# Performance work log

Hardware: AMD Instinct MI355X
Metric: run time of the kernel (lower is better)

## Reference

```python
import jax, jax.numpy as jnp
import numpy as np

B, L, DM, H, DH = 2, 2048, 1024, 4, 128
TOT = H * DH  # 512


def _dwconv(x, w, b, L):
    # x: (B,L,C), w: (C,1,4) depthwise, padding=3 then causal trim to L (matches Conv1d(padding=3)[...,:L])
    y = jax.lax.conv_general_dilated(x.transpose(0, 2, 1), w, (1,), [(3, 3)],
                                     dimension_numbers=('NCH', 'OIH', 'NCH'),
                                     feature_group_count=w.shape[0])
    y = y[..., :L] + b[None, :, None]
    return y.transpose(0, 2, 1)


def _l2norm(x):
    return x / jnp.maximum(jnp.linalg.norm(x, axis=-1, keepdims=True), 1e-12)


def setup_inputs() -> dict:
    key = jax.random.key(0)
    ks = jax.random.split(key, 16)
    s = 0.02
    return {
        'x': jax.random.normal(ks[0], (B, L, DM), jnp.float32),
        'state': jnp.zeros((B, H, DH, DH), jnp.float32),
        'Wq': jax.random.normal(ks[1], (TOT, DM), jnp.float32) * s,
        'Wk': jax.random.normal(ks[2], (TOT, DM), jnp.float32) * s,
        'Wv': jax.random.normal(ks[3], (2 * TOT, DM), jnp.float32) * s,
        'Wa': jax.random.normal(ks[4], (H, DM), jnp.float32) * s,
        'Wb': jax.random.normal(ks[5], (H, DM), jnp.float32) * s,
        'Wg': jax.random.normal(ks[6], (TOT, DM), jnp.float32) * s,
        'Wo': jax.random.normal(ks[7], (DM, TOT), jnp.float32) * s,
        'qcw': jax.random.normal(ks[8], (TOT, 1, 4), jnp.float32) * 0.1,
        'qcb': jnp.zeros((TOT,), jnp.float32),
        'kcw': jax.random.normal(ks[9], (TOT, 1, 4), jnp.float32) * 0.1,
        'kcb': jnp.zeros((TOT,), jnp.float32),
        'vcw': jax.random.normal(ks[10], (2 * TOT, 1, 4), jnp.float32) * 0.1,
        'vcb': jnp.zeros((2 * TOT,), jnp.float32),
        'ln_w': jnp.ones((TOT,), jnp.float32),
        'ln_b': jnp.zeros((TOT,), jnp.float32),
    }


def reference(x, state, Wq, Wk, Wv, Wa, Wb, Wg, Wo, qcw, qcb, kcw, kcb, vcw, vcb, ln_w, ln_b):
    Bn, Ln, _ = x.shape
    q = _dwconv(x @ Wq.T, qcw, qcb, Ln)
    k = _dwconv(x @ Wk.T, kcw, kcb, Ln)
    v = _dwconv(x @ Wv.T, vcw, vcb, Ln)
    # silu then L2-normalize over the FULL total_dim (before head split), as in the source
    q = _l2norm(jax.nn.silu(q))
    k = _l2norm(jax.nn.silu(k))
    v = jax.nn.silu(v)
    alpha = jax.nn.sigmoid(x @ Wa.T)  # (B,L,H)
    beta = jax.nn.sigmoid(x @ Wb.T)   # (B,L,H)
    q = q.reshape(Bn, Ln, H, DH)
    k = k.reshape(Bn, Ln, H, DH)
    v_main, v_gate = jnp.split(v, 2, axis=-1)
    v_main = v_main.reshape(Bn, Ln, H, DH)
    v_gate = v_gate.reshape(Bn, Ln, H, DH)

    def step(S, inp):
        q_t, k_t, v_t, a_t, b_t = inp  # (B,H,D),(B,H,D),(B,H,D),(B,H),(B,H)
        a = a_t[..., None, None]
        b = b_t[..., None, None]
        Sk = jnp.einsum('bhij,bhj->bhi', S, k_t)  # S @ k
        # S @ (alpha*(I - beta k k^T)) + beta v k^T, via rank-1 update
        S = a * (S - b * (Sk[..., :, None] * k_t[..., None, :])) \
            + b * (v_t[..., :, None] * k_t[..., None, :])
        o = jnp.einsum('bhij,bhj->bhi', S, q_t)
        return S, o

    xs = (q.transpose(1, 0, 2, 3), k.transpose(1, 0, 2, 3), v_main.transpose(1, 0, 2, 3),
          alpha.transpose(1, 0, 2), beta.transpose(1, 0, 2))
    final_state, outs = jax.lax.scan(step, state, xs)
    out = outs.transpose(1, 0, 2, 3)  # (B,L,H,D)

    out = (out * v_gate).reshape(Bn, Ln, TOT)
    out = out * jax.nn.silu(x @ Wg.T)
    mu = out.mean(-1, keepdims=True)
    var = jnp.mean((out - mu) ** 2, axis=-1, keepdims=True)
    out = (out - mu) * jax.lax.rsqrt(var + 1e-5) * ln_w + ln_b
    out = out @ Wo.T
    return out, final_state
```

## Files before the change

### kernel.cpp

```cpp
#include <hip/hip_runtime.h>
#include <hip/hip_bf16.h>

#define BQ    2
#define LQ    2048
#define DMQ   1024
#define HQ    4
#define DHQ   128
#define TOTQ  512
#define BLQ   4096
#define NPROJ 2688
#define KPROJ 1024
#define CT    64
#define NCH   32

typedef short bf16x8 __attribute__((ext_vector_type(8)));
typedef short s16x4  __attribute__((ext_vector_type(4)));
typedef float f32x4  __attribute__((ext_vector_type(4)));

#define MFMA16(a, b, c) __builtin_amdgcn_mfma_f32_16x16x32_bf16(a, b, c, 0, 0, 0)

__device__ __forceinline__ float siluf(float x) { return x / (1.f + __expf(-x)); }
__device__ __forceinline__ float sigf(float x)  { return 1.f / (1.f + __expf(-x)); }
__device__ __forceinline__ short bf16s(float x) {
  return __builtin_bit_cast(short, __float2bfloat16(x));
}
__device__ __forceinline__ float bfu2f(unsigned short u) {
  return __bfloat162float(__builtin_bit_cast(__hip_bfloat16, u));
}
__device__ __forceinline__ bf16x8 pack8(f32x4 a, f32x4 b) {
  bf16x8 r;
  r[0] = bf16s(a.x); r[1] = bf16s(a.y); r[2] = bf16s(a.z); r[3] = bf16s(a.w);
  r[4] = bf16s(b.x); r[5] = bf16s(b.y); r[6] = bf16s(b.z); r[7] = bf16s(b.w);
  return r;
}

__device__ __forceinline__ void gload_lds16(const void* g, void* l) {
  __builtin_amdgcn_global_load_lds(
      (__attribute__((address_space(1))) void*)(unsigned long long)g,
      (__attribute__((address_space(3))) void*)(unsigned int)(unsigned long long)l,
      16, 0, 0);
}

__global__ __launch_bounds__(256)
void cast_all_kernel(const float* __restrict__ x, const float* __restrict__ Wo,
                     const float* __restrict__ Wq, const float* __restrict__ Wk,
                     const float* __restrict__ Wv, const float* __restrict__ Wg,
                     const float* __restrict__ Wa, const float* __restrict__ Wb,
                     __hip_bfloat16* __restrict__ XB, __hip_bfloat16* __restrict__ WOB,
                     __hip_bfloat16* __restrict__ Wcat)
{
  const int bid = blockIdx.x;
  const int tid = threadIdx.x;
  if (bid < 4096) {
    const int i = bid * 256 + tid;
    float4 v = ((const float4*)x)[i];
    __hip_bfloat16 o[4] = { __float2bfloat16(v.x), __float2bfloat16(v.y),
                            __float2bfloat16(v.z), __float2bfloat16(v.w) };
    *(ushort4*)((unsigned short*)XB + (size_t)i * 4) = *(ushort4*)o;
  } else if (bid < 4608) {
    const int i = (bid - 4096) * 256 + tid;
    float4 v = ((const float4*)Wo)[i];
    __hip_bfloat16 o[4] = { __float2bfloat16(v.x), __float2bfloat16(v.y),
                            __float2bfloat16(v.z), __float2bfloat16(v.w) };
    *(ushort4*)((unsigned short*)WOB + (size_t)i * 4) = *(ushort4*)o;
  } else {
    const int i4 = (bid - 4608) * 256 + tid;
    const int row = i4 >> 8;
    const int col = (i4 & 255) * 4;
    const int idx = row * 1024 + col;
    float4 v;
    if      (row < 512)  v = *(const float4*)(Wq + idx);
    else if (row < 1024) v = *(const float4*)(Wk + idx - 512 * 1024);
    else if (row < 2048) v = *(const float4*)(Wv + idx - 1024 * 1024);
    else if (row < 2560) v = *(const float4*)(Wg + idx - 2048 * 1024);
    else if (row < 2564) v = *(const float4*)(Wa + (row - 2560) * 1024 + col);
    else if (row < 2568) v = *(const float4*)(Wb + (row - 2564) * 1024 + col);
    else                 v = make_float4(0.f, 0.f, 0.f, 0.f);
    __hip_bfloat16 o[4] = { __float2bfloat16(v.x), __float2bfloat16(v.y),
                            __float2bfloat16(v.z), __float2bfloat16(v.w) };
    *(ushort4*)((unsigned short*)Wcat + idx) = *(ushort4*)o;
  }
}

template <typename TOUT>
__global__ __launch_bounds__(256)
void gemm_bt_kernel(const __hip_bfloat16* __restrict__ A,
                    const __hip_bfloat16* __restrict__ Bw,
                    TOUT* __restrict__ C, int M, int N, int K,
                    float* __restrict__ aux, int auxc0)
{
  __shared__ __hip_bfloat16 As[2 * 128 * 32];
  __shared__ __hip_bfloat16 Bs[2 * 128 * 32];
  const int tid  = threadIdx.x;
  const int lane = tid & 63;
  const int w    = tid >> 6;
  const int wm   = w >> 1, wn = w & 1;
  const int tm   = blockIdx.x, tn = blockIdx.y;
  const int lr   = lane & 15, lk = lane >> 4;

  f32x4 acc[4][4] = {};

  const int e0   = tid * 8;
  const int srow = e0 >> 5;
  const int scol = e0 & 31;
  const __hip_bfloat16* Ap = A  + (size_t)(tm * 128 + srow) * K + scol;
  const __hip_bfloat16* Bp = Bw + (size_t)(tn * 128 + srow) * K + scol;
  char* AsB  = (char*)As;
  char* BsB  = (char*)Bs;
  const size_t half = (size_t)64 * K;
  const int nk = K >> 5;

  {
    char* AsD = AsB + w * 1024;
    char* BsD = BsB + w * 1024;
    gload_lds16(Ap,        AsD);
    gload_lds16(Ap + half, AsD + 4096);
    gload_lds16(Bp,        BsD);
    gload_lds16(Bp + half, BsD + 4096);
  }
  __syncthreads();

  for (int it = 0; it < nk; ++it) {
    const int sel = it & 1;
    if (it + 1 < nk) {
      const int kk = (it + 1) * 32;
      char* AsD = AsB + ((sel ^ 1) * 8192) + w * 1024;
      char* BsD = BsB + ((sel ^ 1) * 8192) + w * 1024;
      gload_lds16(Ap + kk,        AsD);
      gload_lds16(Ap + half + kk, AsD + 4096);
      gload_lds16(Bp + kk,        BsD);
      gload_lds16(Bp + half + kk, BsD + 4096);
    }
    const char* AsR = AsB + sel * 8192;
    const char* BsR = BsB + sel * 8192;
    bf16x8 af[4], bfv[4];
#pragma unroll
    for (int m = 0; m < 4; ++m)
      af[m]  = *(const bf16x8*)(AsR + ((wm * 64 + m * 16 + lr) * 32 + lk * 8) * 2);
#pragma unroll
    for (int n = 0; n < 4; ++n)
      bfv[n] = *(const bf16x8*)(BsR + ((wn * 64 + n * 16 + lr) * 32 + lk * 8) * 2);
#pragma unroll
    for (int m = 0; m < 4; ++m)
#pragma unroll
      for (int n = 0; n < 4; ++n)
        acc[m][n] = MFMA16(af[m], bfv[n], acc[m][n]);
    __syncthreads();
  }

  const int crow0 = tm * 128 + wm * 64 + (lane >> 4) * 4;
  const int ccol0 = tn * 128 + wn * 64 + lr;
#pragma unroll
  for (int m = 0; m < 4; ++m)
#pragma unroll
    for (int n = 0; n < 4; ++n) {
      const int cc = ccol0 + n * 16;
#pragma unroll
      for (int j = 0; j < 4; ++j) {
        const float v = acc[m][n][j];
        const size_t row = (size_t)(crow0 + m * 16 + j);
        if constexpr (sizeof(TOUT) == 2)
          ((unsigned short*)C)[row * N + cc] = (unsigned short)bf16s(v);
        else
          C[row * N + cc] = v;
        if (aux && cc >= auxc0 && cc < auxc0 + 8)
          aux[row * 8 + (cc - auxc0)] = v;
      }
    }
}

__global__ __launch_bounds__(256)
void conv_act_kernel(const __hip_bfloat16* __restrict__ C, const float* __restrict__ abf,
                     const float* __restrict__ qcw, const float* __restrict__ qcb,
                     const float* __restrict__ kcw, const float* __restrict__ kcb,
                     const float* __restrict__ vcw, const float* __restrict__ vcb,
                     __hip_bfloat16* __restrict__ qh, __hip_bfloat16* __restrict__ kh,
                     __hip_bfloat16* __restrict__ vm, __hip_bfloat16* __restrict__ vg,
                     float* __restrict__ al, float* __restrict__ be)
{
  const int blk = blockIdx.x;
  const int bl0 = blk * 8;
  const int t0  = bl0 & (LQ - 1);
  const int tid = threadIdx.x;
  const unsigned short* Cu = (const unsigned short*)C;
  __shared__ float red[4][16];

  float2 qv[8], kv[8];
  float sq[8], sk[8];
#pragma unroll
  for (int t = 0; t < 8; ++t) { sq[t] = 0.f; sk[t] = 0.f; }

  {
    const int c0 = tid * 2;
    const float4 wqA = *(const float4*)(qcw + 4 * c0);
    const float4 wqB = *(const float4*)(qcw + 4 * c0 + 4);
    const float4 wkA = *(const float4*)(kcw + 4 * c0);
    const float4 wkB = *(const float4*)(kcw + 4 * c0 + 4);
    const float2 bq = *(const float2*)(qcb + c0);
    const float2 bk = *(const float2*)(kcb + c0);
    float2 wrq[11], wrk[11];
#pragma unroll
    for (int r = 0; r < 11; ++r) {
      const int tt = t0 - 3 + r;
      if (tt >= 0) {
        const unsigned short* Cr = Cu + (size_t)(bl0 - 3 + r) * NPROJ;
        const ushort2 aq = *(const ushort2*)(Cr + c0);
        const ushort2 ak = *(const ushort2*)(Cr + 512 + c0);
        wrq[r] = make_float2(bfu2f(aq.x), bfu2f(aq.y));
        wrk[r] = make_float2(bfu2f(ak.x), bfu2f(ak.y));
      } else {
        wrq[r] = make_float2(0.f, 0.f);
        wrk[r] = make_float2(0.f, 0.f);
      }
    }
#pragma unroll
    for (int t = 0; t < 8; ++t) {
      float aq0 = bq.x, aq1 = bq.y, ak0 = bk.x, ak1 = bk.y;
#pragma unroll
      for (int j = 0; j < 4; ++j) {
        aq0 = fmaf(((const float*)&wqA)[j], wrq[t + j].x, aq0);
        aq1 = fmaf(((const float*)&wqB)[j], wrq[t + j].y, aq1);
        ak0 = fmaf(((const float*)&wkA)[j], wrk[t + j].x, ak0);
        ak1 = fmaf(((const float*)&wkB)[j], wrk[t + j].y, ak1);
      }
      const float q0 = siluf(aq0), q1 = siluf(aq1);
      const float k0 = siluf(ak0), k1 = siluf(ak1);
      qv[t] = make_float2(q0, q1);
      kv[t] = make_float2(k0, k1);
      sq[t] = fmaf(q1, q1, fmaf(q0, q0, sq[t]));
      sk[t] = fmaf(k1, k1, fmaf(k0, k0, sk[t]));
    }
  }
#pragma unroll
  for (int m = 1; m < 64; m <<= 1) {
#pragma unroll
    for (int t = 0; t < 8; ++t) {
      sq[t] += __shfl_xor(sq[t], m);
      sk[t] += __shfl_xor(sk[t], m);
    }
  }
  {
    const int w = tid >> 6, lane = tid & 63;
    if (lane == 0) {
#pragma unroll
      for (int t = 0; t < 8; ++t) { red[w][t] = sq[t]; red[w][8 + t] = sk[t]; }
    }
  }
  __syncthreads();
  float rnq[8], rnk[8];
#pragma unroll
  for (int t = 0; t < 8; ++t) {
    const float SQ = red[0][t] + red[1][t] + red[2][t] + red[3][t];
    const float SK = red[0][8 + t] + red[1][8 + t] + red[2][8 + t] + red[3][8 + t];
    rnq[t] = 1.f / fmaxf(sqrtf(SQ), 1e-12f);
    rnk[t] = 1.f / fmaxf(sqrtf(SK), 1e-12f);
  }
  {
    const int c0 = tid * 2;
#pragma unroll
    for (int t = 0; t < 8; ++t) {
      ushort2 oq, ok;
      oq.x = (unsigned short)bf16s(qv[t].x * rnq[t]);
      oq.y = (unsigned short)bf16s(qv[t].y * rnq[t]);
      ok.x = (unsigned short)bf16s(kv[t].x * rnk[t]);
      ok.y = (unsigned short)bf16s(kv[t].y * rnk[t]);
      *(ushort2*)((unsigned short*)qh + (size_t)(bl0 + t) * 512 + c0) = oq;
      *(ushort2*)((unsigned short*)kh + (size_t)(bl0 + t) * 512 + c0) = ok;
    }
  }
  {
    const int cv = tid * 4;
    const float4 wv0 = *(const float4*)(vcw + 4 * cv);
    const float4 wv1 = *(const float4*)(vcw + 4 * cv + 4);
    const float4 wv2 = *(const float4*)(vcw + 4 * cv + 8);
    const float4 wv3 = *(const float4*)(vcw + 4 * cv + 12);
    const float4 bv4 = *(const float4*)(vcb + cv);
    float4 wr[11];
#pragma unroll
    for (int r = 0; r < 11; ++r) {
      const int tt = t0 - 3 + r;
      if (tt >= 0) {
        const ushort4 u = *(const ushort4*)(Cu + (size_t)(bl0 - 3 + r) * NPROJ + 1024 + cv);
        wr[r] = make_float4(bfu2f(u.x), bfu2f(u.y), bfu2f(u.z), bfu2f(u.w));
      } else {
        wr[r] = make_float4(0.f, 0.f, 0.f, 0.f);
      }
    }
#pragma unroll
    for (int t = 0; t < 8; ++t) {
      float a0 = bv4.x, a1 = bv4.y, a2 = bv4.z, a3 = bv4.w;
#pragma unroll
      for (int j = 0; j < 4; ++j) {
        a0 = fmaf(((const float*)&wv0)[j], ((const float*)&wr[t + j])[0], a0);
        a1 = fmaf(((const float*)&wv1)[j], ((const float*)&wr[t + j])[1], a1);
        a2 = fmaf(((const float*)&wv2)[j], ((const float*)&wr[t + j])[2], a2);
        a3 = fmaf(((const float*)&wv3)[j], ((const float*)&wr[t + j])[3], a3);
      }
      ushort4 o;
      o.x = (unsigned short)bf16s(siluf(a0));
      o.y = (unsigned short)bf16s(siluf(a1));
      o.z = (unsigned short)bf16s(siluf(a2));
      o.w = (unsigned short)bf16s(siluf(a3));
      if (cv < 512) *(ushort4*)((unsigned short*)vm + (size_t)(bl0 + t) * 512 + cv)         = o;
      else          *(ushort4*)((unsigned short*)vg + (size_t)(bl0 + t) * 512 + (cv - 512)) = o;
    }
  }
  if (tid < 64) {
    const int t = tid >> 3;
    const int k = tid & 7;
    const float v = abf[(size_t)(bl0 + t) * 8 + k];
    if (k < 4) al[(size_t)(bl0 + t) * 4 + k]       = sigf(v);
    else       be[(size_t)(bl0 + t) * 4 + (k - 4)] = sigf(v);
  }
}

__global__ __launch_bounds__(512)
void scan_phaseA_kernel(const __hip_bfloat16* __restrict__ qh, const __hip_bfloat16* __restrict__ kh,
                        const __hip_bfloat16* __restrict__ vm, const float* __restrict__ al,
                        const float* __restrict__ be,
                        short* __restrict__ WTB, short* __restrict__ ZB,
                        short* __restrict__ PHB, float* __restrict__ GV,
                        short* __restrict__ TRB, float* __restrict__ BF)
{
  __shared__ char sm[136192];
  float* Xl = (float*)(sm);
  __hip_bfloat16* KBl = (__hip_bfloat16*)(sm);
  __hip_bfloat16* QBl = (__hip_bfloat16*)(sm + 17408);
  float* Ll  = (float*)(sm + 65536);
  float* dv  = (float*)(sm + 82944);
  float* bv  = (float*)(sm + 83200);
  float* gbv = (float*)(sm + 83456);
  float* fvs = (float*)(sm + 83712);
  short* KTl  = (short*)(sm + 83968);
  short* WTFl = (short*)(sm + 101376);
  short* ZFl  = (short*)(sm + 118784);

  const int cb = blockIdx.x;
  const int bh = cb & 7, c = cb >> 3;
  const int b = bh >> 2, h = bh & 3;
  const int tid = threadIdx.x;
  const int lane = tid & 63;
  const int w = tid >> 6;
  const int lr = lane & 15, lk = lane >> 4;
  const size_t rowbase = (size_t)(b * LQ + c * CT) * 512 + h * 128;

#pragma unroll
  for (int rep = 0; rep < 2; ++rep) {
    const int fid = tid + rep * 512;
    const int r = fid >> 4;
    const int cg = (fid & 15) * 8;
    *(bf16x8*)(KBl + r * 136 + cg) = *(const bf16x8*)(kh + rowbase + (size_t)r * 512 + cg);
    *(bf16x8*)(QBl + r * 136 + cg) = *(const bf16x8*)(qh + rowbase + (size_t)r * 512 + cg);
  }
  if (w == 0) {
    float la = __logf(al[(size_t)(b * LQ + c * CT + lane) * 4 + h]);
    const float bb = be[(size_t)(b * LQ + c * CT + lane) * 4 + h];
#pragma unroll
    for (int off = 1; off < 64; off <<= 1) {
      const float tv = __shfl_up(la, off, 64);
      if (lane >= off) la += tv;
    }
    dv[lane] = la; bv[lane] = bb; gbv[lane] = bb * __expf(la);
    const float d63 = __shfl(la, 63, 64);
    fvs[lane] = __expf(d63 - la);
    GV[cb * 64 + lane] = __expf(la);
  }
  __syncthreads();

  {
    const int tb = (w & 3) * 16;
    const int sh = (w >> 2) * 2;
    f32x4 aG[2] = {}, aP[2] = {};
#pragma unroll
    for (int ks = 0; ks < 4; ++ks) {
      bf16x8 bk[2];
#pragma unroll
      for (int nt = 0; nt < 2; ++nt)
        bk[nt] = *(const bf16x8*)(KBl + ((sh + nt) * 16 + lr) * 136 + ks * 32 + lk * 8);
      const bf16x8 ak = *(const bf16x8*)(KBl + (tb + lr) * 136 + ks * 32 + lk * 8);
      const bf16x8 aq = *(const bf16x8*)(QBl + (tb + lr) * 136 + ks * 32 + lk * 8);
#pragma unroll
      for (int nt = 0; nt < 2; ++nt) {
        aG[nt] = MFMA16(ak, bk[nt], aG[nt]);
        aP[nt] = MFMA16(aq, bk[nt], aP[nt]);
      }
    }
#pragma unroll
    for (int nt = 0; nt < 2; ++nt)
#pragma unroll
      for (int jj = 0; jj < 4; ++jj) {
        const int t = tb + lk * 4 + jj;
        const int s = (sh + nt) * 16 + lr;
        const float eg = __expf(dv[t] - dv[s]);
        Ll[t * 68 + s] = (t > s) ? bv[t] * eg * aG[nt][jj] : 0.f;
        PHB[(size_t)cb * 4096 + t * 64 + s] = (s <= t) ? bf16s(eg * aP[nt][jj]) : (short)0;
      }
  }
  if (tid < 128) {
    const short* Kbs = (const short*)KBl;
#pragma unroll
    for (int s4 = 0; s4 < 16; ++s4) {
      s16x4 pk;
#pragma unroll
      for (int e = 0; e < 4; ++e)
        pk[e] = Kbs[(s4 * 4 + e) * 136 + tid];
      *(s16x4*)(KTl + tid * 68 + s4 * 4) = pk;
    }
  }
  __syncthreads();

  const int j = tid & 255;
  const int half = tid >> 8;
  const int i0 = half * 8;
  const __hip_bfloat16* src = (j < 128) ? kh : vm;
  const __hip_bfloat16* xp = src + rowbase + (j & 127);
  float* XlC = Xl + j;
  short* dstN = (j < 128) ? (WTB + (size_t)cb * 8192 + j)
                          : (ZB  + (size_t)cb * 8192 + (j - 128));
  short* dstT = (j < 128) ? (WTFl + j * 68)
                          : (ZFl  + (j - 128) * 68);

  for (int r = 0; r < 4; ++r) {
    float u[8];
#pragma unroll
    for (int i = 0; i < 8; ++i) {
      const int t = r * 16 + i0 + i;
      u[i] = __bfloat162float(xp[(size_t)t * 512]) * ((j < 128) ? gbv[t] : bv[t]);
    }
    for (int sc = 0; sc < r; ++sc) {
      float xs[16];
#pragma unroll
      for (int k = 0; k < 16; ++k) xs[k] = XlC[(sc * 16 + k) * 256];
#pragma unroll
      for (int i = 0; i < 8; ++i) {
        const float* lrow = Ll + (r * 16 + i0 + i) * 68 + sc * 16;
        const f32x4 l0 = *(const f32x4*)(lrow);
        const f32x4 l1 = *(const f32x4*)(lrow + 4);
        const f32x4 l2 = *(const f32x4*)(lrow + 8);
        const f32x4 l3 = *(const f32x4*)(lrow + 12);
        f32x4 acc = {};
        acc.x = fmaf(l0.x, xs[0],  acc.x); acc.y = fmaf(l0.y, xs[1],  acc.y);
        acc.z = fmaf(l0.z, xs[2],  acc.z); acc.w = fmaf(l0.w, xs[3],  acc.w);
        acc.x = fmaf(l1.x, xs[4],  acc.x); acc.y = fmaf(l1.y, xs[5],  acc.y);
        acc.z = fmaf(l1.z, xs[6],  acc.z); acc.w = fmaf(l1.w, xs[7],  acc.w);
        acc.x = fmaf(l2.x, xs[8],  acc.x); acc.y = fmaf(l2.y, xs[9],  acc.y);
        acc.z = fmaf(l2.z, xs[10], acc.z); acc.w = fmaf(l2.w, xs[11], acc.w);
        acc.x = fmaf(l3.x, xs[12], acc.x); acc.y = fmaf(l3.y, xs[13], acc.y);
        acc.z = fmaf(l3.z, xs[14], acc.z); acc.w = fmaf(l3.w, xs[15], acc.w);
        u[i] -= (acc.x + acc.y) + (acc.z + acc.w);
      }
    }
    if (half == 0) {
#pragma unroll
      for (int i = 1; i < 8; ++i) {
        const float* lrow = Ll + (r * 16 + i) * 68 + r * 16;
        f32x4 acc = {};
#pragma unroll
        for (int k4 = 0; k4 < 2; ++k4) {
          if (k4 * 4 < i) {
            const f32x4 lv = *(const f32x4*)(lrow + k4 * 4);
            acc.x = fmaf(lv.x, u[k4 * 4 + 0], acc.x);
            acc.y = fmaf(lv.y, u[k4 * 4 + 1], acc.y);
            acc.z = fmaf(lv.z, u[k4 * 4 + 2], acc.z);
            acc.w = fmaf(lv.w, u[k4 * 4 + 3], acc.w);
          }
        }
        u[i] -= (acc.x + acc.y) + (acc.z + acc.w);
      }
#pragma unroll
      for (int i = 0; i < 8; ++i) XlC[(r * 16 + i) * 256] = u[i];
#pragma unroll
      for (int i = 0; i < 8; ++i) dstN[(r * 16 + i) * 128] = bf16s(u[i]);
#pragma unroll
      for (int s4 = 0; s4 < 2; ++s4) {
        s16x4 p;
#pragma unroll
        for (int e = 0; e < 4; ++e)
          p[e] = bf16s(fvs[r * 16 + s4 * 4 + e] * u[s4 * 4 + e]);
        *(s16x4*)(dstT + r * 16 + s4 * 4) = p;
      }
    }
    __syncthreads();
    if (half == 1) {
      float xa[8];
#pragma unroll
      for (int k = 0; k < 8; ++k) xa[k] = XlC[(r * 16 + k) * 256];
#pragma unroll
      for (int i = 0; i < 8; ++i) {
        const float* lrow = Ll + (r * 16 + 8 + i) * 68 + r * 16;
        const f32x4 l0 = *(const f32x4*)(lrow);
        const f32x4 l1 = *(const f32x4*)(lrow + 4);
        f32x4 acc = {};
        acc.x = fmaf(l0.x, xa[0], acc.x); acc.y = fmaf(l0.y, xa[1], acc.y);
        acc.z = fmaf(l0.z, xa[2], acc.z); acc.w = fmaf(l0.w, xa[3], acc.w);
        acc.x = fmaf(l1.x, xa[4], acc.x); acc.y = fmaf(l1.y, xa[5], acc.y);
        acc.z = fmaf(l1.z, xa[6], acc.z); acc.w = fmaf(l1.w, xa[7], acc.w);
        u[i] -= (acc.x + acc.y) + (acc.z + acc.w);
      }
#pragma unroll
      for (int i = 1; i < 8; ++i) {
        const float* lrow = Ll + (r * 16 + 8 + i) * 68 + r * 16 + 8;
        f32x4 acc = {};
#pragma unroll
        for (int k4 = 0; k4 < 2; ++k4) {
          if (k4 * 4 < i) {
            const f32x4 lv = *(const f32x4*)(lrow + k4 * 4);
            acc.x = fmaf(lv.x, u[k4 * 4 + 0], acc.x);
            acc.y = fmaf(lv.y, u[k4 * 4 + 1], acc.y);
            acc.z = fmaf(lv.z, u[k4 * 4 + 2], acc.z);
            acc.w = fmaf(lv.w, u[k4 * 4 + 3], acc.w);
          }
        }
        u[i] -= (acc.x + acc.y) + (acc.z + acc.w);
      }
#pragma unroll
      for (int i = 0; i < 8; ++i) XlC[(r * 16 + 8 + i) * 256] = u[i];
#pragma unroll
      for (int i = 0; i < 8; ++i) dstN[(r * 16 + 8 + i) * 128] = bf16s(u[i]);
#pragma unroll
      for (int s4 = 0; s4 < 2; ++s4) {
        s16x4 p;
#pragma unroll
        for (int e = 0; e < 4; ++e)
          p[e] = bf16s(fvs[r * 16 + 8 + s4 * 4 + e] * u[s4 * 4 + e]);
        *(s16x4*)(dstT + r * 16 + 8 + s4 * 4) = p;
      }
    }
    __syncthreads();
  }

  const float gc = __expf(dv[63]);
  const int rb = (w & 3) * 32;
  const int cq = (w >> 2) * 4;
  {
    f32x4 acc[2][4] = {};
#pragma unroll
    for (int ks = 0; ks < 2; ++ks) {
      const bf16x8 a0 = *(const bf16x8*)(KTl + (rb + lr) * 68 + ks * 32 + lk * 8);
      const bf16x8 a1 = *(const bf16x8*)(KTl + (rb + 16 + lr) * 68 + ks * 32 + lk * 8);
#pragma unroll
      for (int nt = 0; nt < 4; ++nt) {
        const bf16x8 bm = *(const bf16x8*)(WTFl + ((cq + nt) * 16 + lr) * 68 + ks * 32 + lk * 8);
        acc[0][nt] = MFMA16(a0, bm, acc[0][nt]);
        acc[1][nt] = MFMA16(a1, bm, acc[1][nt]);
      }
    }
#pragma unroll
    for (int mt = 0; mt < 2; ++mt)
#pragma unroll
      for (int nt = 0; nt < 4; ++nt)
#pragma unroll
        for (int jj = 0; jj < 4; ++jj) {
          const int jr = rb + mt * 16 + lk * 4 + jj;
          const int m  = (cq + nt) * 16 + lr;
          const float v = ((jr == m) ? gc : 0.f) - acc[mt][nt][jj];
          TRB[(size_t)cb * 16384 + jr * 128 + m] = bf16s(v);
        }
  }
  {
    f32x4 acc[2][4] = {};
#pragma unroll
    for (int ks = 0; ks < 2; ++ks) {
      const bf16x8 a0 = *(const bf16x8*)(ZFl + (rb + lr) * 68 + ks * 32 + lk * 8);
      const bf16x8 a1 = *(const bf16x8*)(ZFl + (rb + 16 + lr) * 68 + ks * 32 + lk * 8);
#pragma unroll
      for (int nt = 0; nt < 4; ++nt) {
        const bf16x8 bj = *(const bf16x8*)(KTl + ((cq + nt) * 16 + lr) * 68 + ks * 32 + lk * 8);
        acc[0][nt] = MFMA16(a0, bj, acc[0][nt]);
        acc[1][nt] = MFMA16(a1, bj, acc[1][nt]);
      }
    }
#pragma unroll
    for (int mt = 0; mt < 2; ++mt)
#pragma unroll
      for (int nt = 0; nt < 4; ++nt)
#pragma unroll
        for (int jj = 0; jj < 4; ++jj) {
          const int ir = rb + mt * 16 + lk * 4 + jj;
          const int jc = (cq + nt) * 16 + lr;
          BF[(size_t)cb * 16384 + ir * 128 + jc] = acc[mt][nt][jj];
        }
  }
}

#define L2_PREFETCH(BT, BA, CC) do {                                               \
  const int cbn_ = (CC) * 8 + bh;                                                  \
  _Pragma("unroll") for (int nt = 0; nt < 2; ++nt) {                               \
    _Pragma("unroll") for (int ks = 0; ks < 4; ++ks)                               \
      BT[nt][ks] = *(const bf16x8*)(TRB + (size_t)cbn_ * 16384 +                   \
                                    (w * 32 + nt * 16 + lr) * 128 + ks * 32 + lk * 8); \
    _Pragma("unroll") for (int jj = 0; jj < 4; ++jj)                               \
      BA[nt][jj] = BF[(size_t)cbn_ * 16384 + (r0 + lk * 4 + jj) * 128 +            \
                      w * 32 + nt * 16 + lr];                                      \
  }                                                                                \
} while (0)

#define L2_STEP(BT, BA, CC, PBT, PBA) do {                                         \
  const int cb_ = (CC) * 8 + bh;                                                   \
  { const int idx = tid * 8, r = idx >> 7, jc = idx & 127;                         \
    f32x4 s0 = *(const f32x4*)&Scur[r * 132 + jc];                                 \
    f32x4 s1 = *(const f32x4*)&Scur[r * 132 + jc + 4];                             \
    *(bf16x8*)(SALL + (size_t)cb_ * 16384 + (r0 + r) * 128 + jc) = pack8(s0, s1); }\
  bf16x8 af[4];                                                                    \
  _Pragma("unroll") for (int ks = 0; ks < 4; ++ks)                                 \
    af[ks] = pack8(*(const f32x4*)&Scur[lr * 132 + ks * 32 + lk * 8],              \
                   *(const f32x4*)&Scur[lr * 132 + ks * 32 + lk * 8 + 4]);         \
  if ((CC) < 31) L2_PREFETCH(PBT, PBA, (CC) + 1);                                  \
  f32x4 acc0 = {}, acc1 = {};                                                      \
  _Pragma("unroll") for (int ks = 0; ks < 4; ++ks) {                               \
    acc0 = MFMA16(af[ks], BT[0][ks], acc0);                                        \
    acc1 = MFMA16(af[ks], BT[1][ks], acc1);                                        \
  }                                                                                \
  _Pragma("unroll") for (int jj = 0; jj < 4; ++jj) {                               \
    Snxt[(lk * 4 + jj) * 132 + w * 32 + lr]      = acc0[jj] + BA[0][jj];           \
    Snxt[(lk * 4 + jj) * 132 + w * 32 + 16 + lr] = acc1[jj] + BA[1][jj];           \
  }                                                                                \
  __syncthreads();                                                                 \
  { float* t_ = Scur; Scur = Snxt; Snxt = t_; }                                    \
} while (0)

__global__ __launch_bounds__(256)
void scan_state_kernel(const short* __restrict__ TRB, const float* __restrict__ BF,
                       const float* __restrict__ st0, short* __restrict__ SALL,
                       float* __restrict__ stout)
{
  __shared__ float Sl[2 * 16 * 132];
  const int bid = blockIdx.x;
  const int bh = bid & 7, slab = bid >> 3;
  const int r0 = slab * 16;
  const int tid = threadIdx.x, lane = tid & 63, w = tid >> 6;
  const int lr = lane & 15, lk = lane >> 4;

  float* Scur = Sl;
  float* Snxt = Sl + 16 * 132;

  {
    const int idx = tid * 8, r = idx >> 7, jc = idx & 127;
    const float* sp = st0 + ((size_t)bh * 128 + r0 + r) * 128 + jc;
    *(f32x4*)&Scur[r * 132 + jc]     = *(const f32x4*)sp;
    *(f32x4*)&Scur[r * 132 + jc + 4] = *(const f32x4*)(sp + 4);
  }
  bf16x8 btA[2][4], btB[2][4];
  float  baA[2][4], baB[2][4];
  L2_PREFETCH(btA, baA, 0);
  __syncthreads();

  for (int c2 = 0; c2 < 16; ++c2) {
    L2_STEP(btA, baA, 2 * c2,     btB, baB);
    L2_STEP(btB, baB, 2 * c2 + 1, btA, baA);
  }

  {
    const int idx = tid * 8, r = idx >> 7, jc = idx & 127;
    float* sp = stout + ((size_t)bh * 128 + r0 + r) * 128 + jc;
    *(f32x4*)sp       = *(const f32x4*)&Scur[r * 132 + jc];
    *(f32x4*)(sp + 4) = *(const f32x4*)&Scur[r * 132 + jc + 4];
  }
}

__global__ __launch_bounds__(512)
void scan_output_kernel(const __hip_bfloat16* __restrict__ qh,
                        const short* __restrict__ WTB, const __hip_bfloat16* __restrict__ ZB,
                        const short* __restrict__ PHB, const float* __restrict__ GV,
                        const short* __restrict__ SALL, __hip_bfloat16* __restrict__ obuf)
{
  __shared__ short Ut[128 * 72];
  const int cb = blockIdx.x;
  const int bh = cb & 7, c = cb >> 3;
  const int b = bh >> 2, h = bh & 3;
  const int tid = threadIdx.x, lane = tid & 63, w = tid >> 6;
  const int lr = lane & 15, lk = lane >> 4;
  const int r0 = (w & 3) * 16;

  f32x4 Y[8] = {};
#pragma unroll
  for (int ks = 0; ks < 4; ++ks) {
    bf16x8 af;
    if (w < 4) {
      af = *(const bf16x8*)(qh + ((size_t)(b * LQ + c * CT) + r0 + lr) * 512 + h * 128 + ks * 32 + lk * 8);
    } else {
      af = *(const bf16x8*)(WTB + (size_t)cb * 8192 + (r0 + lr) * 128 + ks * 32 + lk * 8);
    }
#pragma unroll
    for (int nt = 0; nt < 8; ++nt) {
      const bf16x8 bs = *(const bf16x8*)(SALL + (size_t)cb * 16384 + (nt * 16 + lr) * 128 + ks * 32 + lk * 8);
      Y[nt] = MFMA16(af, bs, Y[nt]);
    }
  }
  if (w >= 4) {
#pragma unroll
    for (int nt = 0; nt < 8; ++nt) {
      const int i = nt * 16 + lr;
      s16x4 up;
#pragma unroll
      for (int jj = 0; jj < 4; ++jj) {
        const int s = r0 + lk * 4 + jj;
        const float z = __bfloat162float(ZB[(size_t)cb * 8192 + s * 128 + i]);
        up[jj] = bf16s(z - Y[nt][jj]);
      }
      *(s16x4*)&Ut[i * 72 + r0 + lk * 4] = up;
    }
  }
  __syncthreads();
  if (w < 4) {
    f32x4 P2[8] = {};
#pragma unroll
    for (int ks = 0; ks < 2; ++ks) {
      const bf16x8 ap = *(const bf16x8*)(PHB + (size_t)cb * 4096 + (r0 + lr) * 64 + ks * 32 + lk * 8);
#pragma unroll
      for (int nt = 0; nt < 8; ++nt) {
        const bf16x8 bu = *(const bf16x8*)&Ut[(nt * 16 + lr) * 72 + ks * 32 + lk * 8];
        P2[nt] = MFMA16(ap, bu, P2[nt]);
      }
    }
    float gvv[4];
#pragma unroll
    for (int jj = 0; jj < 4; ++jj) gvv[jj] = GV[cb * 64 + r0 + lk * 4 + jj];
#pragma unroll
    for (int nt = 0; nt < 8; ++nt) {
      const int i = nt * 16 + lr;
#pragma unroll
      for (int jj = 0; jj < 4; ++jj) {
        const int t = r0 + lk * 4 + jj;
        ((unsigned short*)obuf)[((size_t)(b * LQ + c * CT) + t) * 512 + h * 128 + i] =
            (unsigned short)bf16s(gvv[jj] * Y[nt][jj] + P2[nt][jj]);
      }
    }
  }
}

__global__ __launch_bounds__(256)
void gate_ln_kernel(const __hip_bfloat16* __restrict__ obuf, const __hip_bfloat16* __restrict__ vg,
                    const __hip_bfloat16* __restrict__ C, const float* __restrict__ lnw,
                    const float* __restrict__ lnb, __hip_bfloat16* __restrict__ lno)
{
  const int bl = blockIdx.x, tid = threadIdx.x;
  const int c0 = tid * 2;
  __shared__ float red[8];
  const ushort2 ovu = *(const ushort2*)((const unsigned short*)obuf + (size_t)bl * 512 + c0);
  const ushort2 gvu = *(const ushort2*)((const unsigned short*)vg + (size_t)bl * 512 + c0);
  const ushort2 ggu = *(const ushort2*)((const unsigned short*)C + (size_t)bl * NPROJ + 2048 + c0);
  const float v0 = bfu2f(ovu.x) * bfu2f(gvu.x) * siluf(bfu2f(ggu.x));
  const float v1 = bfu2f(ovu.y) * bfu2f(gvu.y) * siluf(bfu2f(ggu.y));
  float s = v0 + v1;
  float s2 = fmaf(v1, v1, v0 * v0);
  float2 pr = make_float2(s, s2);
#pragma unroll
  for (int m = 1; m < 64; m <<= 1) { pr.x += __shfl_xor(pr.x, m); pr.y += __shfl_xor(pr.y, m); }
  if ((tid & 63) == 0) { red[(tid >> 6) * 2] = pr.x; red[(tid >> 6) * 2 + 1] = pr.y; }
  __syncthreads();
  const float S  = red[0] + red[2] + red[4] + red[6];
  const float S2 = red[1] + red[3] + red[5] + red[7];
  const float mu  = S * (1.f / 512.f);
  const float var = S2 * (1.f / 512.f) - mu * mu;
  const float rs  = rsqrtf(var + 1e-5f);
  const float2 lw = *(const float2*)(lnw + c0);
  const float2 lb = *(const float2*)(lnb + c0);
  __hip_bfloat16 o[2] = {
    __float2bfloat16(fmaf((v0 - mu) * rs, lw.x, lb.x)),
    __float2bfloat16(fmaf((v1 - mu) * rs, lw.y, lb.y)) };
  *(ushort2*)((unsigned short*)lno + (size_t)bl * 512 + c0) = *(ushort2*)o;
}

extern "C" void kernel_launch(void* const* d_in, const int* in_sizes, int n_in,
                              void* d_out, int out_size, void* d_ws, size_t ws_size,
                              hipStream_t stream)
{
  (void)in_sizes; (void)n_in; (void)out_size; (void)ws_size;
  const float* x    = (const float*)d_in[0];
  const float* st0  = (const float*)d_in[1];
  const float* Wq   = (const float*)d_in[2];
  const float* Wk   = (const float*)d_in[3];
  const float* Wv   = (const float*)d_in[4];
  const float* Wa   = (const float*)d_in[5];
  const float* Wb   = (const float*)d_in[6];
  const float* Wg   = (const float*)d_in[7];
  const float* Wo   = (const float*)d_in[8];
  const float* qcw  = (const float*)d_in[9];
  const float* qcb  = (const float*)d_in[10];
  const float* kcw  = (const float*)d_in[11];
  const float* kcb  = (const float*)d_in[12];
  const float* vcw  = (const float*)d_in[13];
  const float* vcb  = (const float*)d_in[14];
  const float* lnw  = (const float*)d_in[15];
  const float* lnb  = (const float*)d_in[16];
  float* out = (float*)d_out;

  char* ws = (char*)d_ws;
  __hip_bfloat16* XB   = (__hip_bfloat16*)(ws + 0);
  __hip_bfloat16* LNO  = (__hip_bfloat16*)(ws + 0);
  short*          WTB  = (short*)(ws + 4194304);
  __hip_bfloat16* WCAT = (__hip_bfloat16*)(ws + 8388608);
  __hip_bfloat16* WOB  = (__hip_bfloat16*)(ws + 13893632);
  __hip_bfloat16* CBUFH = (__hip_bfloat16*)(ws + 14942208);
  __hip_bfloat16* QH   = (__hip_bfloat16*)(ws + 58982400);
  __hip_bfloat16* KH   = (__hip_bfloat16*)(ws + 67371008);
  __hip_bfloat16* VM   = (__hip_bfloat16*)(ws + 75759616);
  __hip_bfloat16* VG   = (__hip_bfloat16*)(ws + 84148224);
  float* AL   = (float*)(ws + 92536832);
  float* BE   = (float*)(ws + 92602368);
  __hip_bfloat16* OBUF = (__hip_bfloat16*)(ws + 92667904);
  short* TRB  = (short*)(ws + 92667904);
  short* PHB  = (short*)(ws + 105250816);
  short* ZB   = (short*)(ws + 107347968);
  float* GV   = (float*)(ws + 111542272);
  short* SALL = (short*)(ws + 115868672);
  float* ABF  = (float*)(ws + 124257280);
  float* BF   = (float*)(ws + 124388352);

  cast_all_kernel<<<7296, 256, 0, stream>>>(x, Wo, Wq, Wk, Wv, Wg, Wa, Wb, XB, WOB, WCAT);

  gemm_bt_kernel<__hip_bfloat16><<<dim3(32, 21), 256, 0, stream>>>(
      XB, WCAT, CBUFH, BLQ, NPROJ, KPROJ, ABF, 2560);

  conv_act_kernel<<<512, 256, 0, stream>>>(CBUFH, ABF, qcw, qcb, kcw, kcb, vcw, vcb,
                                           QH, KH, VM, VG, AL, BE);

  scan_phaseA_kernel<<<256, 512, 0, stream>>>(QH, KH, VM, AL, BE,
                                              WTB, ZB, PHB, GV, TRB, BF);

  scan_state_kernel<<<64, 256, 0, stream>>>(TRB, BF, st0, SALL, out + 4194304);

  scan_output_kernel<<<256, 512, 0, stream>>>(QH, WTB, (const __hip_bfloat16*)ZB,
                                              PHB, GV, SALL, OBUF);

  gate_ln_kernel<<<BLQ, 256, 0, stream>>>(OBUF, VG, CBUFH, lnw, lnb, LNO);

  gemm_bt_kernel<float><<<dim3(32, 8), 256, 0, stream>>>(
      LNO, WOB, out, BLQ, DMQ, TOTQ, nullptr, 0);
}
```

Before: 143.5 us.

## Widen GEMM tiles to 128x256 with 512 threads and XCD-aware block remap

The projection and output GEMMs now use 128x256 output tiles computed by 8 waves, with a 1D grid and a block-index remap that groups consecutive tiles per XCD. NPROJ is padded to 2816 so it divides by 256, and the workspace offsets are packed more tightly. The aim is more B-operand reuse per tile and better L2 locality. In exchange, the grid has fewer blocks (128 for the output GEMM, which may underfill 256 CUs), uses more LDS, and pads more weight rows.

New measurement: 149.6 us. 1.04x slower.

```diff
diff --git a/kernel.cpp b/kernel.cpp
--- a/kernel.cpp
+++ b/kernel.cpp
@@ -8,7 +8,7 @@
 #define DHQ   128
 #define TOTQ  512
 #define BLQ   4096
-#define NPROJ 2688
+#define NPROJ 2816
 #define KPROJ 1024
 #define CT    64
 #define NCH   32
@@ -83,40 +83,40 @@
 }
 
 template <typename TOUT>
-__global__ __launch_bounds__(256)
+__global__ __launch_bounds__(512)
 void gemm_bt_kernel(const __hip_bfloat16* __restrict__ A,
                     const __hip_bfloat16* __restrict__ Bw,
                     TOUT* __restrict__ C, int M, int N, int K,
                     float* __restrict__ aux, int auxc0)
 {
   __shared__ __hip_bfloat16 As[2 * 128 * 32];
-  __shared__ __hip_bfloat16 Bs[2 * 128 * 32];
+  __shared__ __hip_bfloat16 Bs[2 * 256 * 32];
   const int tid  = threadIdx.x;
   const int lane = tid & 63;
   const int w    = tid >> 6;
-  const int wm   = w >> 1, wn = w & 1;
-  const int tm   = blockIdx.x, tn = blockIdx.y;
+  const int wm   = w >> 2, wn = w & 3;
+  const int nwg  = gridDim.x;
+  const int bid  = blockIdx.x;
+  const int wgid = (bid & 7) * (nwg >> 3) + (bid >> 3);
+  const int tm   = wgid & 31;
+  const int tn   = wgid >> 5;
   const int lr   = lane & 15, lk = lane >> 4;
 
   f32x4 acc[4][4] = {};
 
-  const int e0   = tid * 8;
-  const int srow = e0 >> 5;
-  const int scol = e0 & 31;
+  const int srow = tid >> 2;
+  const int scol = (tid & 3) * 8;
   const __hip_bfloat16* Ap = A  + (size_t)(tm * 128 + srow) * K + scol;
-  const __hip_bfloat16* Bp = Bw + (size_t)(tn * 128 + srow) * K + scol;
+  const __hip_bfloat16* Bp = Bw + (size_t)(tn * 256 + srow) * K + scol;
+  const size_t halfB = (size_t)128 * K;
   char* AsB  = (char*)As;
   char* BsB  = (char*)Bs;
-  const size_t half = (size_t)64 * K;
   const int nk = K >> 5;
 
   {
-    char* AsD = AsB + w * 1024;
-    char* BsD = BsB + w * 1024;
-    gload_lds16(Ap,        AsD);
-    gload_lds16(Ap + half, AsD + 4096);
-    gload_lds16(Bp,        BsD);
-    gload_lds16(Bp + half, BsD + 4096);
+    gload_lds16(Ap,         AsB + w * 1024);
+    gload_lds16(Bp,         BsB + w * 1024);
+    gload_lds16(Bp + halfB, BsB + 8192 + w * 1024);
   }
   __syncthreads();
 
@@ -124,15 +124,12 @@
     const int sel = it & 1;
     if (it + 1 < nk) {
       const int kk = (it + 1) * 32;
-      char* AsD = AsB + ((sel ^ 1) * 8192) + w * 1024;
-      char* BsD = BsB + ((sel ^ 1) * 8192) + w * 1024;
-      gload_lds16(Ap + kk,        AsD);
-      gload_lds16(Ap + half + kk, AsD + 4096);
-      gload_lds16(Bp + kk,        BsD);
-      gload_lds16(Bp + half + kk, BsD + 4096);
+      gload_lds16(Ap + kk,         AsB + ((sel ^ 1) * 8192)  + w * 1024);
+      gload_lds16(Bp + kk,         BsB + ((sel ^ 1) * 16384) + w * 1024);
+      gload_lds16(Bp + halfB + kk, BsB + ((sel ^ 1) * 16384) + 8192 + w * 1024);
     }
     const char* AsR = AsB + sel * 8192;
-    const char* BsR = BsB + sel * 8192;
+    const char* BsR = BsB + sel * 16384;
     bf16x8 af[4], bfv[4];
 #pragma unroll
     for (int m = 0; m < 4; ++m)
@@ -148,8 +145,8 @@
     __syncthreads();
   }
 
-  const int crow0 = tm * 128 + wm * 64 + (lane >> 4) * 4;
-  const int ccol0 = tn * 128 + wn * 64 + lr;
+  const int crow0 = tm * 128 + wm * 64 + lk * 4;
+  const int ccol0 = tn * 256 + wn * 64 + lr;
 #pragma unroll
   for (int m = 0; m < 4; ++m)
 #pragma unroll
@@ -791,26 +788,26 @@
   __hip_bfloat16* LNO  = (__hip_bfloat16*)(ws + 0);
   short*          WTB  = (short*)(ws + 4194304);
   __hip_bfloat16* WCAT = (__hip_bfloat16*)(ws + 8388608);
-  __hip_bfloat16* WOB  = (__hip_bfloat16*)(ws + 13893632);
-  __hip_bfloat16* CBUFH = (__hip_bfloat16*)(ws + 14942208);
-  __hip_bfloat16* QH   = (__hip_bfloat16*)(ws + 58982400);
-  __hip_bfloat16* KH   = (__hip_bfloat16*)(ws + 67371008);
-  __hip_bfloat16* VM   = (__hip_bfloat16*)(ws + 75759616);
-  __hip_bfloat16* VG   = (__hip_bfloat16*)(ws + 84148224);
-  float* AL   = (float*)(ws + 92536832);
-  float* BE   = (float*)(ws + 92602368);
-  __hip_bfloat16* OBUF = (__hip_bfloat16*)(ws + 92667904);
-  short* TRB  = (short*)(ws + 92667904);
-  short* PHB  = (short*)(ws + 105250816);
-  short* ZB   = (short*)(ws + 107347968);
-  float* GV   = (float*)(ws + 111542272);
-  short* SALL = (short*)(ws + 115868672);
-  float* ABF  = (float*)(ws + 124257280);
-  float* BF   = (float*)(ws + 124388352);
-
-  cast_all_kernel<<<7296, 256, 0, stream>>>(x, Wo, Wq, Wk, Wv, Wg, Wa, Wb, XB, WOB, WCAT);
-
-  gemm_bt_kernel<__hip_bfloat16><<<dim3(32, 21), 256, 0, stream>>>(
+  __hip_bfloat16* WOB  = (__hip_bfloat16*)(ws + 14155776);
+  __hip_bfloat16* CBUFH = (__hip_bfloat16*)(ws + 15204352);
+  __hip_bfloat16* QH   = (__hip_bfloat16*)(ws + 38273024);
+  __hip_bfloat16* KH   = (__hip_bfloat16*)(ws + 42467328);
+  __hip_bfloat16* VM   = (__hip_bfloat16*)(ws + 46661632);
+  __hip_bfloat16* VG   = (__hip_bfloat16*)(ws + 50855936);
+  float* AL   = (float*)(ws + 55050240);
+  float* BE   = (float*)(ws + 55115776);
+  __hip_bfloat16* OBUF = (__hip_bfloat16*)(ws + 55181312);
+  short* TRB  = (short*)(ws + 55181312);
+  short* PHB  = (short*)(ws + 63569920);
+  short* ZB   = (short*)(ws + 65667072);
+  float* GV   = (float*)(ws + 69861376);
+  short* SALL = (short*)(ws + 69926912);
+  float* ABF  = (float*)(ws + 78315520);
+  float* BF   = (float*)(ws + 78446592);
+
+  cast_all_kernel<<<7424, 256, 0, stream>>>(x, Wo, Wq, Wk, Wv, Wg, Wa, Wb, XB, WOB, WCAT);
+
+  gemm_bt_kernel<__hip_bfloat16><<<352, 512, 0, stream>>>(
       XB, WCAT, CBUFH, BLQ, NPROJ, KPROJ, ABF, 2560);
 
   conv_act_kernel<<<512, 256, 0, stream>>>(CBUFH, ABF, qcw, qcb, kcw, kcb, vcw, vcb,
@@ -826,6 +823,6 @@
 
   gate_ln_kernel<<<BLQ, 256, 0, stream>>>(OBUF, VG, CBUFH, lnw, lnb, LNO);
 
-  gemm_bt_kernel<float><<<dim3(32, 8), 256, 0, stream>>>(
+  gemm_bt_kernel<float><<<128, 512, 0, stream>>>(
       LNO, WOB, out, BLQ, DMQ, TOTQ, nullptr, 0);
 }
```
